# Performance work log

Hardware: AMD Instinct MI355X
Metric: run time of the kernel (lower is better)

## Reference

```python
import math
import jax, jax.numpy as jnp
import numpy as np

L, D, H, F = 4, 1024, 16, 4096
HD = D // H
EPS = 1e-5


def get_alibi_slopes(num_heads):
    closest = 2 ** math.floor(math.log2(num_heads))
    base = 2 ** (-2 ** (-(math.log2(closest) - 3)))
    slopes = base ** np.arange(1, closest + 1)
    if closest != num_heads:
        extra_base = 2 ** (-2 ** (-(math.log2(2 * closest) - 3)))
        extra = extra_base ** np.arange(1, 2 * (num_heads - closest) + 1, 2)
        slopes = np.concatenate([slopes, extra])
    return jnp.asarray(slopes, dtype=jnp.float32)


def build_mask(num_heads, T):
    # causal: -inf above diagonal; plus ALiBi slopes * (key_pos - query_pos)
    pos = jnp.arange(T)
    dist = pos[None, :] - pos[:, None]                      # (T, T)
    alibi = get_alibi_slopes(num_heads)[:, None, None] * dist[None]  # (H, T, T)
    causal = jnp.where(dist > 0, -jnp.inf, 0.0).astype(jnp.float32)
    return causal[None] + alibi                             # (H, T, T)


def layer_norm(x, w, b):
    mu = jnp.mean(x, axis=-1, keepdims=True)
    var = jnp.mean(jnp.square(x - mu), axis=-1, keepdims=True)
    return (x - mu) * jax.lax.rsqrt(var + EPS) * w + b


def mha(x, mask, Wi, bi, Wo, bo):
    B, T, _ = x.shape
    qkv = x @ Wi.T + bi                                     # (B, T, 3D)
    q, k, v = jnp.split(qkv, 3, axis=-1)
    q = q.reshape(B, T, H, HD).transpose(0, 2, 1, 3)        # (B, H, T, hd)
    k = k.reshape(B, T, H, HD).transpose(0, 2, 1, 3)
    v = v.reshape(B, T, H, HD).transpose(0, 2, 1, 3)
    scores = jnp.einsum('bhqd,bhkd->bhqk', q, k) / math.sqrt(HD)
    scores = scores + mask[None]                            # (B, H, T, T)
    attn = jax.nn.softmax(scores, axis=-1)
    out = jnp.einsum('bhqk,bhkd->bhqd', attn, v)
    out = out.transpose(0, 2, 1, 3).reshape(B, T, D)
    return out @ Wo.T + bo


def setup_inputs() -> dict:
    key = jax.random.key(0)
    ks = jax.random.split(key, 13)
    s = 0.02
    inp = {
        'x': jax.random.normal(ks[0], (2, 2048, D), dtype=jnp.float32),
        'in_proj_w': jax.random.normal(ks[1], (L, 3 * D, D), dtype=jnp.float32) * s,
        'in_proj_b': jnp.zeros((L, 3 * D), dtype=jnp.float32),
        'out_proj_w': jax.random.normal(ks[2], (L, D, D), dtype=jnp.float32) * s,
        'out_proj_b': jnp.zeros((L, D), dtype=jnp.float32),
        'ffn1_w': jax.random.normal(ks[3], (L, F, D), dtype=jnp.float32) * s,
        'ffn1_b': jnp.zeros((L, F), dtype=jnp.float32),
        'ffn2_w': jax.random.normal(ks[4], (L, D, F), dtype=jnp.float32) * s,
        'ffn2_b': jnp.zeros((L, D), dtype=jnp.float32),
        'ln1_w': jnp.ones((L, D), dtype=jnp.float32),
        'ln1_b': jnp.zeros((L, D), dtype=jnp.float32),
        'ln2_w': jnp.ones((L, D), dtype=jnp.float32),
        'ln2_b': jnp.zeros((L, D), dtype=jnp.float32),
        'final_w': jnp.ones((D,), dtype=jnp.float32),
        'final_b': jnp.zeros((D,), dtype=jnp.float32),
    }
    return inp


def reference(x, in_proj_w, in_proj_b, out_proj_w, out_proj_b,
              ffn1_w, ffn1_b, ffn2_w, ffn2_b,
              ln1_w, ln1_b, ln2_w, ln2_b, final_w, final_b):
    T = x.shape[1]
    mask = build_mask(H, T)                                 # (H, T, T)
    for i in range(L):
        xn = layer_norm(x, ln1_w[i], ln1_b[i])
        x = x + mha(xn, mask, in_proj_w[i], in_proj_b[i], out_proj_w[i], out_proj_b[i])
        xn = layer_norm(x, ln2_w[i], ln2_b[i])
        h = jax.nn.gelu(xn @ ffn1_w[i].T + ffn1_b[i], approximate=False)
        x = x + (h @ ffn2_w[i].T + ffn2_b[i])
    return layer_norm(x, final_w, final_b)
```

## Files before the change

kernel.cpp:

```cpp
#include <hip/hip_runtime.h>
#include <hip/hip_bf16.h>
#include <math.h>

typedef __bf16 bf16x8 __attribute__((ext_vector_type(8)));
typedef __bf16 bf16x4 __attribute__((ext_vector_type(4)));
typedef float  floatx4 __attribute__((ext_vector_type(4)));

#define D_MODEL 1024
#define SEQ     2048
#define NHEAD   16
#define HD      64

__device__ __forceinline__ void async16(const void* g, void* l) {
  __builtin_amdgcn_global_load_lds((const __attribute__((address_space(1))) void*)g,
                                   (__attribute__((address_space(3))) void*)l, 16, 0, 0);
}

__global__ __launch_bounds__(256)
void cvtw_kernel(const float* __restrict__ in, __bf16* __restrict__ out) {
  const size_t i = ((size_t)blockIdx.x * 256 + threadIdx.x) * 4;
  const floatx4 f = *(const floatx4*)(in + i);
  bf16x4 o = { (__bf16)f[0], (__bf16)f[1], (__bf16)f[2], (__bf16)f[3] };
  *(bf16x4*)(out + i) = o;
}

template<bool OUT_BF16>
__global__ __launch_bounds__(256)
void ln_kernel(const float* __restrict__ x, const float* __restrict__ w,
               const float* __restrict__ b, void* __restrict__ out)
{
  const int row = blockIdx.x;
  const int tid = threadIdx.x;
  const floatx4 f = *(const floatx4*)(x + (size_t)row * D_MODEL + tid * 4);
  float s = f[0] + f[1] + f[2] + f[3];
  #pragma unroll
  for (int off = 1; off < 64; off <<= 1) s += __shfl_xor(s, off);
  __shared__ float red[8];
  const int wv = tid >> 6;
  if ((tid & 63) == 0) red[wv] = s;
  __syncthreads();
  const float mu = (red[0] + red[1] + red[2] + red[3]) * (1.0f / 1024.0f);
  float d0 = f[0] - mu, d1 = f[1] - mu, d2 = f[2] - mu, d3 = f[3] - mu;
  float ss = d0 * d0 + d1 * d1 + d2 * d2 + d3 * d3;
  #pragma unroll
  for (int off = 1; off < 64; off <<= 1) ss += __shfl_xor(ss, off);
  if ((tid & 63) == 0) red[4 + wv] = ss;
  __syncthreads();
  const float rstd = rsqrtf((red[4] + red[5] + red[6] + red[7]) * (1.0f / 1024.0f) + 1e-5f);
  const floatx4 wv4 = *(const floatx4*)(w + tid * 4);
  const floatx4 bv4 = *(const floatx4*)(b + tid * 4);
  const float y0 = d0 * rstd * wv4[0] + bv4[0];
  const float y1 = d1 * rstd * wv4[1] + bv4[1];
  const float y2 = d2 * rstd * wv4[2] + bv4[2];
  const float y3 = d3 * rstd * wv4[3] + bv4[3];
  if (OUT_BF16) {
    bf16x4 o = { (__bf16)y0, (__bf16)y1, (__bf16)y2, (__bf16)y3 };
    *(bf16x4*)((__bf16*)out + (size_t)row * D_MODEL + tid * 4) = o;
  } else {
    floatx4 o = { y0, y1, y2, y3 };
    *(floatx4*)((float*)out + (size_t)row * D_MODEL + tid * 4) = o;
  }
}

#define EPI_GELU 1
#define EPI_RES  2
#define EPI_QKV  3

__device__ __forceinline__ void stage_tile(const __bf16* Ab, const __bf16* Wb,
                                           int K, int k0,
                                           __bf16 (*As)[64], __bf16 (*Bs)[64], int tid)
{
  #pragma unroll
  for (int j = 0; j < 4; ++j) {
    const int ch = j * 512 + tid;
    const int row = ch >> 3, c16 = ch & 7;
    const int gc = (c16 ^ (row & 7)) * 8;
    async16(Ab + (size_t)row * K + k0 + gc, &As[row][c16 * 8]);
  }
  #pragma unroll
  for (int j = 0; j < 4; ++j) {
    const int ch = j * 512 + tid;
    const int row = ch >> 3, c16 = ch & 7;
    const int gc = (c16 ^ (row & 7)) * 8;
    async16(Wb + (size_t)row * K + k0 + gc, &Bs[row][c16 * 8]);
  }
}

template<int MODE>
__global__ __launch_bounds__(512, 2)
void gemm256_kernel(const __bf16* __restrict__ A, const __bf16* __restrict__ W,
                    const float* __restrict__ bias, void* out,
                    __bf16* __restrict__ vT, int M, int N, int K)
{
  __shared__ __align__(16) __bf16 As[2][256][64];
  __shared__ __align__(16) __bf16 Bs[2][256][64];
  const int tid = threadIdx.x;
  const int lane = tid & 63, wv = tid >> 6;
  const int wr = wv >> 2, wc = wv & 3;
  const int quad = lane >> 4, r = lane & 15;
  const int sw = r & 7;
  const int m0 = blockIdx.x * 256, n0 = blockIdx.y * 256;
  const __bf16* Ab = A + (size_t)m0 * K;
  const __bf16* Wb = W + (size_t)n0 * K;

  floatx4 acc[8][4] = {};

  const int nt = K >> 6;
  stage_tile(Ab, Wb, K, 0, As[0], Bs[0], tid);

  for (int t = 0; t < nt; ++t) {
    const int p = t & 1;
    const int kn = (t + 1 < nt) ? ((t + 1) << 6) : 0;
    stage_tile(Ab, Wb, K, kn, As[p ^ 1], Bs[p ^ 1], tid);
    asm volatile("s_waitcnt vmcnt(8)" ::: "memory");
    __builtin_amdgcn_s_barrier();
    asm volatile("" ::: "memory");
    __bf16 (*Asr)[64] = As[p];
    __bf16 (*Bsr)[64] = Bs[p];
    #pragma unroll
    for (int kk = 0; kk < 2; ++kk) {
      const int cc = ((kk * 4 + quad) ^ sw) * 8;
      bf16x8 av[8], bv[4];
      #pragma unroll
      for (int mi = 0; mi < 8; ++mi)
        av[mi] = *(const bf16x8*)&Asr[wr * 128 + mi * 16 + r][cc];
      #pragma unroll
      for (int ni = 0; ni < 4; ++ni)
        bv[ni] = *(const bf16x8*)&Bsr[wc * 64 + ni * 16 + r][cc];
      __builtin_amdgcn_s_setprio(1);
      #pragma unroll
      for (int ni = 0; ni < 4; ++ni)
        #pragma unroll
        for (int mi = 0; mi < 8; ++mi)
          acc[mi][ni] = __builtin_amdgcn_mfma_f32_16x16x32_bf16(
              av[mi], bv[ni], acc[mi][ni], 0, 0, 0);
      __builtin_amdgcn_s_setprio(0);
    }
    asm volatile("" ::: "memory");
    __builtin_amdgcn_s_barrier();
  }
  asm volatile("s_waitcnt vmcnt(0)" ::: "memory");

  #pragma unroll
  for (int ni = 0; ni < 4; ++ni) {
    const int nn = n0 + wc * 64 + ni * 16 + r;
    const float bvv = bias[nn];
    #pragma unroll
    for (int mi = 0; mi < 8; ++mi) {
      #pragma unroll
      for (int v = 0; v < 4; ++v) {
        const int mm = m0 + wr * 128 + mi * 16 + quad * 4 + v;
        float val = acc[mi][ni][v] + bvv;
        if (MODE == EPI_GELU) {
          val = 0.5f * val * (1.0f + erff(val * 0.70710678118654752f));
          ((__bf16*)out)[(size_t)mm * N + nn] = (__bf16)val;
        } else if (MODE == EPI_QKV) {
          if (nn < 2048) {
            const float sv = (nn < 1024) ? val * 0.125f : val;
            ((__bf16*)out)[(size_t)mm * 2048 + nn] = (__bf16)sv;
          } else {
            const int c = nn - 2048, hh = c >> 6, dd = c & 63;
            const int bb = mm >> 11, tt = mm & 2047;
            vT[(size_t)((bb * 16 + hh) * 64 + dd) * 2048 + tt] = (__bf16)val;
          }
        }
      }
    }
  }
}

__global__ __launch_bounds__(256, 2)
void gemm64_kernel(const __bf16* __restrict__ A, const __bf16* __restrict__ W,
                   const float* __restrict__ bias, float* __restrict__ out,
                   const float* __restrict__ res, int M, int N, int K)
{
  __shared__ __align__(16) __bf16 As0[128][32], As1[128][32];
  __shared__ __align__(16) __bf16 Ws0[64][32],  Ws1[64][32];
  const int tid = threadIdx.x;
  const int lane = tid & 63, w = tid >> 6;
  const int wr = w >> 1, wc = w & 1;
  const int quad = lane >> 4, r = lane & 15;
  const int m0 = blockIdx.x * 128, n0 = blockIdx.y * 64;

  floatx4 acc[4][2] = {};

  const __bf16* Ab = A + (size_t)m0 * K;
  const __bf16* Wb = W + (size_t)n0 * K;
  const int sr = tid >> 2, sc = (tid & 3) * 8;

  for (int k0 = 0; k0 < K; k0 += 64) {
    async16(Ab + (size_t)sr * K + k0 + sc,             &As0[sr][sc]);
    async16(Ab + (size_t)(sr + 64) * K + k0 + sc,      &As0[sr + 64][sc]);
    async16(Ab + (size_t)sr * K + k0 + 32 + sc,        &As1[sr][sc]);
    async16(Ab + (size_t)(sr + 64) * K + k0 + 32 + sc, &As1[sr + 64][sc]);
    async16(Wb + (size_t)sr * K + k0 + sc,             &Ws0[sr][sc]);
    async16(Wb + (size_t)sr * K + k0 + 32 + sc,        &Ws1[sr][sc]);
    __syncthreads();
    bf16x8 af0[4], af1[4];
    #pragma unroll
    for (int mi = 0; mi < 4; ++mi) {
      af0[mi] = *(const bf16x8*)&As0[wr * 64 + mi * 16 + r][quad * 8];
      af1[mi] = *(const bf16x8*)&As1[wr * 64 + mi * 16 + r][quad * 8];
    }
    #pragma unroll
    for (int ni = 0; ni < 2; ++ni) {
      const bf16x8 b0 = *(const bf16x8*)&Ws0[wc * 32 + ni * 16 + r][quad * 8];
      const bf16x8 b1 = *(const bf16x8*)&Ws1[wc * 32 + ni * 16 + r][quad * 8];
      #pragma unroll
      for (int mi = 0; mi < 4; ++mi) {
        acc[mi][ni] = __builtin_amdgcn_mfma_f32_16x16x32_bf16(af0[mi], b0, acc[mi][ni], 0, 0, 0);
        acc[mi][ni] = __builtin_amdgcn_mfma_f32_16x16x32_bf16(af1[mi], b1, acc[mi][ni], 0, 0, 0);
      }
    }
    __syncthreads();
  }

  #pragma unroll
  for (int ni = 0; ni < 2; ++ni) {
    const int nn = n0 + wc * 32 + ni * 16 + r;
    const float bv = bias[nn];
    #pragma unroll
    for (int mi = 0; mi < 4; ++mi) {
      #pragma unroll
      for (int v = 0; v < 4; ++v) {
        const int mm = m0 + wr * 64 + mi * 16 + quad * 4 + v;
        out[(size_t)mm * N + nn] = res[(size_t)mm * N + nn] + acc[mi][ni][v] + bv;
      }
    }
  }
}

template<int MODE, int NT>
__global__ __launch_bounds__(256, 2)
void gemm_legacy_kernel(const __bf16* __restrict__ A, const float* __restrict__ W,
                        const float* __restrict__ bias, void* out,
                        const float* __restrict__ res, __bf16* __restrict__ vT,
                        int M, int N, int K)
{
  __shared__ __align__(16) __bf16 As[128][32];
  __shared__ __align__(16) __bf16 Ws[NT][32];
  const int tid = threadIdx.x;
  const int lane = tid & 63, w = tid >> 6;
  const int wr = w >> 1, wc = w & 1;
  const int quad = lane >> 4, r = lane & 15;
  constexpr int NACC = NT / 32;
  const int m0 = blockIdx.x * 128, n0 = blockIdx.y * NT;
  floatx4 acc[4][NACC] = {};
  const __bf16* Ab = A + (size_t)m0 * K;
  const float*  Wb = W + (size_t)n0 * K;
  const int arow = tid >> 2, ac = (tid & 3) * 8;
  const int wrow = tid >> 3, wc4 = (tid & 7) * 4;
  for (int k0 = 0; k0 < K; k0 += 32) {
    async16(Ab + (size_t)arow * K + k0 + ac, &As[arow][ac]);
    async16(Ab + (size_t)(arow + 64) * K + k0 + ac, &As[arow + 64][ac]);
    #pragma unroll
    for (int i = 0; i < NT / 32; ++i) {
      const int rw = wrow + 32 * i;
      const floatx4 f = *(const floatx4*)(Wb + (size_t)rw * K + k0 + wc4);
      bf16x4 h4 = { (__bf16)f[0], (__bf16)f[1], (__bf16)f[2], (__bf16)f[3] };
      *(bf16x4*)&Ws[rw][wc4] = h4;
    }
    __syncthreads();
    bf16x8 af[4];
    #pragma unroll
    for (int mi = 0; mi < 4; ++mi)
      af[mi] = *(const bf16x8*)&As[wr * 64 + mi * 16 + r][quad * 8];
    #pragma unroll
    for (int ni = 0; ni < NACC; ++ni) {
      bf16x8 bf = *(const bf16x8*)&Ws[wc * (NT / 2) + ni * 16 + r][quad * 8];
      #pragma unroll
      for (int mi = 0; mi < 4; ++mi)
        acc[mi][ni] = __builtin_amdgcn_mfma_f32_16x16x32_bf16(af[mi], bf, acc[mi][ni], 0, 0, 0);
    }
    __syncthreads();
  }
  #pragma unroll
  for (int ni = 0; ni < NACC; ++ni) {
    const int nn = n0 + wc * (NT / 2) + ni * 16 + r;
    const float bv = bias[nn];
    #pragma unroll
    for (int mi = 0; mi < 4; ++mi) {
      #pragma unroll
      for (int v = 0; v < 4; ++v) {
        const int mm = m0 + wr * 64 + mi * 16 + quad * 4 + v;
        float val = acc[mi][ni][v] + bv;
        if (MODE == EPI_GELU) {
          val = 0.5f * val * (1.0f + erff(val * 0.70710678118654752f));
          ((__bf16*)out)[(size_t)mm * N + nn] = (__bf16)val;
        } else if (MODE == EPI_RES) {
          ((float*)out)[(size_t)mm * N + nn] = res[(size_t)mm * N + nn] + val;
        } else if (MODE == EPI_QKV) {
          if (nn < 2048) {
            const float sv = (nn < 1024) ? val * 0.125f : val;
            ((__bf16*)out)[(size_t)mm * 2048 + nn] = (__bf16)sv;
          } else {
            const int c = nn - 2048, hh = c >> 6, dd = c & 63;
            const int bb = mm >> 11, t = mm & 2047;
            vT[(size_t)((bb * 16 + hh) * 64 + dd) * 2048 + t] = (__bf16)val;
          }
        }
      }
    }
  }
}

__global__ __launch_bounds__(256, 4)
void attn_kernel(const __bf16* __restrict__ qk,
                 const __bf16* __restrict__ vT,
                 __bf16* __restrict__ out)
{
  __shared__ __align__(16) __bf16 Qs[2][64][32];
  __shared__ __align__(16) __bf16 Ks[2][64][32];
  __shared__ __align__(16) __bf16 Vs[2][64][32];
  __shared__ __align__(16) __bf16 Ps[4][2][16][32];
  const int tid = threadIdx.x, lane = tid & 63, w = tid >> 6;
  const int quad = lane >> 4, r = lane & 15;
  const int bh = blockIdx.x, b = bh >> 4, h = bh & 15;
  const int yk = blockIdx.y >> 3, yj = blockIdx.y & 7;
  const int qt = (yk << 3) | ((yk & 1) ? (7 - yj) : yj);
  const int q0 = qt * 64;

  {
    const __bf16* qb = qk + ((size_t)(b * SEQ + q0)) * 2048 + h * 64;
    #pragma unroll
    for (int rd = 0; rd < 2; ++rd) {
      const int c = rd * 256 + tid, half = c >> 8, row = (c >> 2) & 63, c8 = (c & 3) * 8;
      async16(qb + (size_t)row * 2048 + half * 32 + c8, &Qs[half][row][c8]);
    }
  }
  __syncthreads();
  const bf16x8 qf0 = *(const bf16x8*)&Qs[0][w * 16 + r][quad * 8];
  const bf16x8 qf1 = *(const bf16x8*)&Qs[1][w * 16 + r][quad * 8];

  const int q = q0 + w * 16 + r;
  float m_i = -INFINITY, l_i = 0.0f;
  floatx4 ot[4] = {};
  const float slope = exp2f(-0.5f * (float)(h + 1));
  const float sq = slope * (float)q;

  const __bf16* kb0 = qk + ((size_t)(b * SEQ)) * 2048 + 1024 + h * 64;
  const __bf16* vb0 = vT + ((size_t)(bh * 64)) * 2048;

  for (int kt = 0; kt <= qt; ++kt) {
    const int kbase = kt << 6;
    #pragma unroll
    for (int rd = 0; rd < 2; ++rd) {
      const int c = rd * 256 + tid, half = c >> 8, row = (c >> 2) & 63, c8 = (c & 3) * 8;
      async16(kb0 + (size_t)(kbase + row) * 2048 + half * 32 + c8, &Ks[half][row][c8]);
    }
    #pragma unroll
    for (int rd = 0; rd < 2; ++rd) {
      const int c = rd * 256 + tid, kb = c >> 8, d = (c >> 2) & 63, c8 = (c & 3) * 8;
      async16(vb0 + (size_t)d * 2048 + kbase + kb * 32 + c8, &Vs[kb][d][c8]);
    }
    __syncthreads();

    floatx4 st[4];
    #pragma unroll
    for (int t = 0; t < 4; ++t) {
      floatx4 z = { 0.0f, 0.0f, 0.0f, 0.0f };
      const bf16x8 kf0 = *(const bf16x8*)&Ks[0][t * 16 + r][quad * 8];
      const bf16x8 kf1 = *(const bf16x8*)&Ks[1][t * 16 + r][quad * 8];
      z = __builtin_amdgcn_mfma_f32_16x16x32_bf16(kf0, qf0, z, 0, 0, 0);
      st[t] = __builtin_amdgcn_mfma_f32_16x16x32_bf16(kf1, qf1, z, 0, 0, 0);
    }
    float mloc = -INFINITY;
    if (kt == qt) {
      #pragma unroll
      for (int t = 0; t < 4; ++t)
        #pragma unroll
        for (int v = 0; v < 4; ++v) {
          const int key = kbase + t * 16 + quad * 4 + v;
          float sv = st[t][v] + slope * (float)key - sq;
          sv = (key <= q) ? sv : -INFINITY;
          st[t][v] = sv;
          mloc = fmaxf(mloc, sv);
        }
    } else {
      #pragma unroll
      for (int t = 0; t < 4; ++t)
        #pragma unroll
        for (int v = 0; v < 4; ++v) {
          const int key = kbase + t * 16 + quad * 4 + v;
          const float sv = st[t][v] + slope * (float)key - sq;
          st[t][v] = sv;
          mloc = fmaxf(mloc, sv);
        }
    }
    mloc = fmaxf(mloc, __shfl_xor(mloc, 16));
    mloc = fmaxf(mloc, __shfl_xor(mloc, 32));
    const float mn = fmaxf(m_i, mloc);
    const float alpha = __expf(m_i - mn);
    m_i = mn;
    float rsum = 0.0f;
    #pragma unroll
    for (int t = 0; t < 4; ++t) {
      bf16x4 p4;
      #pragma unroll
      for (int v = 0; v < 4; ++v) {
        const float p = __expf(st[t][v] - mn);
        rsum += p;
        p4[v] = (__bf16)p;
      }
      *(bf16x4*)&Ps[w][t >> 1][r][(t & 1) * 16 + quad * 4] = p4;
    }
    rsum += __shfl_xor(rsum, 16);
    rsum += __shfl_xor(rsum, 32);
    l_i = l_i * alpha + rsum;
    #pragma unroll
    for (int dt = 0; dt < 4; ++dt) ot[dt] *= alpha;

    #pragma unroll
    for (int kb = 0; kb < 2; ++kb) {
      const bf16x8 pf = *(const bf16x8*)&Ps[w][kb][r][quad * 8];
      #pragma unroll
      for (int dt = 0; dt < 4; ++dt) {
        const bf16x8 vf = *(const bf16x8*)&Vs[kb][dt * 16 + r][quad * 8];
        ot[dt] = __builtin_amdgcn_mfma_f32_16x16x32_bf16(vf, pf, ot[dt], 0, 0, 0);
      }
    }
    __syncthreads();
  }

  const float linv = 1.0f / l_i;
  __bf16* ob = out + (size_t)(b * SEQ + q) * D_MODEL + h * 64;
  #pragma unroll
  for (int dt = 0; dt < 4; ++dt) {
    bf16x4 o4 = { (__bf16)(ot[dt][0] * linv), (__bf16)(ot[dt][1] * linv),
                  (__bf16)(ot[dt][2] * linv), (__bf16)(ot[dt][3] * linv) };
    *(bf16x4*)(ob + dt * 16 + quad * 4) = o4;
  }
}

extern "C" void kernel_launch(void* const* d_in, const int* in_sizes, int n_in,
                              void* d_out, int out_size, void* d_ws, size_t ws_size,
                              hipStream_t stream)
{
  (void)in_sizes; (void)n_in; (void)out_size;
  const float* x    = (const float*)d_in[0];
  const float* inW  = (const float*)d_in[1];
  const float* inB  = (const float*)d_in[2];
  const float* outW = (const float*)d_in[3];
  const float* outB = (const float*)d_in[4];
  const float* f1W  = (const float*)d_in[5];
  const float* f1B  = (const float*)d_in[6];
  const float* f2W  = (const float*)d_in[7];
  const float* f2B  = (const float*)d_in[8];
  const float* ln1W = (const float*)d_in[9];
  const float* ln1B = (const float*)d_in[10];
  const float* ln2W = (const float*)d_in[11];
  const float* ln2B = (const float*)d_in[12];
  const float* fnW  = (const float*)d_in[13];
  const float* fnB  = (const float*)d_in[14];

  char* ws = (char*)d_ws;
  float*  x_cur = (float*)(ws);
  __bf16* xn    = (__bf16*)(ws + 16777216);
  __bf16* qk    = (__bf16*)(ws + 25165824);
  __bf16* vT    = (__bf16*)(ws + 41943040);
  __bf16* attn  = (__bf16*)(ws + 50331648);
  __bf16* hbuf  = (__bf16*)(ws + 25165824);
  __bf16* inWb  = (__bf16*)(ws + 58720256);
  __bf16* outWb = (__bf16*)(ws + 83886080);
  __bf16* f1Wb  = (__bf16*)(ws + 92274688);
  __bf16* f2Wb  = (__bf16*)(ws + 125829120);
  const bool bf16w = ws_size >= (size_t)159383552;

  hipMemcpyAsync(x_cur, x, (size_t)16777216, hipMemcpyDeviceToDevice, stream);

  if (bf16w) {
    cvtw_kernel<<<dim3(12288), dim3(256), 0, stream>>>(inW,  inWb);
    cvtw_kernel<<<dim3(4096),  dim3(256), 0, stream>>>(outW, outWb);
    cvtw_kernel<<<dim3(16384), dim3(256), 0, stream>>>(f1W,  f1Wb);
    cvtw_kernel<<<dim3(16384), dim3(256), 0, stream>>>(f2W,  f2Wb);
  }

  for (int i = 0; i < 4; ++i) {
    ln_kernel<true><<<dim3(4096), dim3(256), 0, stream>>>(
        x_cur, ln1W + i * 1024, ln1B + i * 1024, xn);
    if (bf16w)
      gemm256_kernel<EPI_QKV><<<dim3(16, 12), dim3(512), 0, stream>>>(
          xn, inWb + (size_t)i * 3072 * 1024, inB + (size_t)i * 3072,
          qk, vT, 4096, 3072, 1024);
    else
      gemm_legacy_kernel<EPI_QKV, 128><<<dim3(32, 24), dim3(256), 0, stream>>>(
          xn, inW + (size_t)i * 3072 * 1024, inB + (size_t)i * 3072,
          qk, nullptr, vT, 4096, 3072, 1024);
    attn_kernel<<<dim3(32, 32), dim3(256), 0, stream>>>(qk, vT, attn);
    if (bf16w)
      gemm64_kernel<<<dim3(32, 16), dim3(256), 0, stream>>>(
          attn, outWb + (size_t)i * 1024 * 1024, outB + (size_t)i * 1024,
          x_cur, x_cur, 4096, 1024, 1024);
    else
      gemm_legacy_kernel<EPI_RES, 64><<<dim3(32, 16), dim3(256), 0, stream>>>(
          attn, outW + (size_t)i * 1024 * 1024, outB + (size_t)i * 1024,
          x_cur, x_cur, nullptr, 4096, 1024, 1024);
    ln_kernel<true><<<dim3(4096), dim3(256), 0, stream>>>(
        x_cur, ln2W + i * 1024, ln2B + i * 1024, xn);
    if (bf16w)
      gemm256_kernel<EPI_GELU><<<dim3(16, 16), dim3(512), 0, stream>>>(
          xn, f1Wb + (size_t)i * 4096 * 1024, f1B + (size_t)i * 4096,
          hbuf, nullptr, 4096, 4096, 1024);
    else
      gemm_legacy_kernel<EPI_GELU, 128><<<dim3(32, 32), dim3(256), 0, stream>>>(
          xn, f1W + (size_t)i * 4096 * 1024, f1B + (size_t)i * 4096,
          hbuf, nullptr, nullptr, 4096, 4096, 1024);
    if (bf16w)
      gemm64_kernel<<<dim3(32, 16), dim3(256), 0, stream>>>(
          hbuf, f2Wb + (size_t)i * 1024 * 4096, f2B + (size_t)i * 1024,
          x_cur, x_cur, 4096, 1024, 4096);
    else
      gemm_legacy_kernel<EPI_RES, 64><<<dim3(32, 16), dim3(256), 0, stream>>>(
          hbuf, f2W + (size_t)i * 1024 * 4096, f2B + (size_t)i * 1024,
          x_cur, x_cur, nullptr, 4096, 1024, 4096);
  }
  ln_kernel<false><<<dim3(4096), dim3(256), 0, stream>>>(x_cur, fnW, fnB, d_out);
}
```

Measured before the change: 1.350 ms.

## Interleave split prefetch with quarter-tile MFMA phases and stage epilogue through LDS

Each K step of the 256x256 bf16 GEMM is split into four MFMA quadrants separated by barriers. The A and W tile prefetches are issued between these phases, so global-to-LDS loads overlap the matrix math and register fragments are reused across quadrants. The epilogue now writes results into LDS and stores coalesced 16-byte vectors, including a transposed staging path for the V output, replacing scattered 2-byte global stores. This adds barriers per K step and per epilogue pass, and relies on syncthreads to make the async loads visible.

```diff
diff --git a/kernel.cpp b/kernel.cpp
--- a/kernel.cpp
+++ b/kernel.cpp
@@ -66,34 +66,16 @@
 #define EPI_RES  2
 #define EPI_QKV  3
 
-__device__ __forceinline__ void stage_tile(const __bf16* Ab, const __bf16* Wb,
-                                           int K, int k0,
-                                           __bf16 (*As)[64], __bf16 (*Bs)[64], int tid)
-{
-  #pragma unroll
-  for (int j = 0; j < 4; ++j) {
-    const int ch = j * 512 + tid;
-    const int row = ch >> 3, c16 = ch & 7;
-    const int gc = (c16 ^ (row & 7)) * 8;
-    async16(Ab + (size_t)row * K + k0 + gc, &As[row][c16 * 8]);
-  }
-  #pragma unroll
-  for (int j = 0; j < 4; ++j) {
-    const int ch = j * 512 + tid;
-    const int row = ch >> 3, c16 = ch & 7;
-    const int gc = (c16 ^ (row & 7)) * 8;
-    async16(Wb + (size_t)row * K + k0 + gc, &Bs[row][c16 * 8]);
-  }
-}
-
 template<int MODE>
 __global__ __launch_bounds__(512, 2)
 void gemm256_kernel(const __bf16* __restrict__ A, const __bf16* __restrict__ W,
                     const float* __restrict__ bias, void* out,
                     __bf16* __restrict__ vT, int M, int N, int K)
 {
-  __shared__ __align__(16) __bf16 As[2][256][64];
-  __shared__ __align__(16) __bf16 Bs[2][256][64];
+  __shared__ __align__(16) char smem[131072];
+  __bf16 (*As)[256][64] = reinterpret_cast<__bf16 (*)[256][64]>(smem);
+  __bf16 (*Bs)[256][64] = reinterpret_cast<__bf16 (*)[256][64]>(smem + 65536);
+
   const int tid = threadIdx.x;
   const int lane = tid & 63, wv = tid >> 6;
   const int wr = wv >> 2, wc = wv & 3;
@@ -106,66 +88,186 @@
   floatx4 acc[8][4] = {};
 
   const int nt = K >> 6;
-  stage_tile(Ab, Wb, K, 0, As[0], Bs[0], tid);
+
+  #pragma unroll
+  for (int j = 0; j < 4; ++j) {
+    const int ch = j * 512 + tid;
+    const int row = ch >> 3, c16 = ch & 7;
+    const int gcb = (c16 ^ (row & 7)) * 8;
+    async16(Ab + (size_t)row * K + gcb, &As[0][row][c16 * 8]);
+  }
+  #pragma unroll
+  for (int j = 0; j < 4; ++j) {
+    const int ch = j * 512 + tid;
+    const int row = ch >> 3, c16 = ch & 7;
+    const int gcb = (c16 ^ (row & 7)) * 8;
+    async16(Wb + (size_t)row * K + gcb, &Bs[0][row][c16 * 8]);
+  }
+  __syncthreads();
 
   for (int t = 0; t < nt; ++t) {
-    const int p = t & 1;
-    const int kn = (t + 1 < nt) ? ((t + 1) << 6) : 0;
-    stage_tile(Ab, Wb, K, kn, As[p ^ 1], Bs[p ^ 1], tid);
-    asm volatile("s_waitcnt vmcnt(8)" ::: "memory");
+    const int pr = t & 1;
+    const __bf16 (*Asr)[64] = As[pr];
+    const __bf16 (*Bsr)[64] = Bs[pr];
+    const bool pf = (t + 1 < nt);
+    const int kn = (t + 1) << 6;
+
+    bf16x8 a0[2][4], b0[2][2], b1[2][2];
+
+    if (pf) {
+      #pragma unroll
+      for (int j = 0; j < 4; ++j) {
+        const int ch = j * 512 + tid;
+        const int row = ch >> 3, c16 = ch & 7;
+        const int gcb = (c16 ^ (row & 7)) * 8;
+        async16(Ab + (size_t)row * K + kn + gcb, &As[pr ^ 1][row][c16 * 8]);
+      }
+    }
+    #pragma unroll
+    for (int kk = 0; kk < 2; ++kk) {
+      const int cc = ((kk * 4 + quad) ^ sw) * 8;
+      #pragma unroll
+      for (int mi = 0; mi < 4; ++mi)
+        a0[kk][mi] = *(const bf16x8*)&Asr[wr * 128 + mi * 16 + r][cc];
+      #pragma unroll
+      for (int ni = 0; ni < 2; ++ni)
+        b0[kk][ni] = *(const bf16x8*)&Bsr[wc * 64 + ni * 16 + r][cc];
+    }
+    __builtin_amdgcn_s_setprio(1);
+    #pragma unroll
+    for (int kk = 0; kk < 2; ++kk)
+      #pragma unroll
+      for (int ni = 0; ni < 2; ++ni)
+        #pragma unroll
+        for (int mi = 0; mi < 4; ++mi)
+          acc[mi][ni] = __builtin_amdgcn_mfma_f32_16x16x32_bf16(
+              a0[kk][mi], b0[kk][ni], acc[mi][ni], 0, 0, 0);
+    __builtin_amdgcn_s_setprio(0);
+    asm volatile("" ::: "memory");
     __builtin_amdgcn_s_barrier();
     asm volatile("" ::: "memory");
-    __bf16 (*Asr)[64] = As[p];
-    __bf16 (*Bsr)[64] = Bs[p];
+
+    if (pf) {
+      #pragma unroll
+      for (int j = 0; j < 4; ++j) {
+        const int ch = j * 512 + tid;
+        const int row = ch >> 3, c16 = ch & 7;
+        const int gcb = (c16 ^ (row & 7)) * 8;
+        async16(Wb + (size_t)row * K + kn + gcb, &Bs[pr ^ 1][row][c16 * 8]);
+      }
+    }
     #pragma unroll
     for (int kk = 0; kk < 2; ++kk) {
       const int cc = ((kk * 4 + quad) ^ sw) * 8;
-      bf16x8 av[8], bv[4];
-      #pragma unroll
-      for (int mi = 0; mi < 8; ++mi)
-        av[mi] = *(const bf16x8*)&Asr[wr * 128 + mi * 16 + r][cc];
-      #pragma unroll
-      for (int ni = 0; ni < 4; ++ni)
-        bv[ni] = *(const bf16x8*)&Bsr[wc * 64 + ni * 16 + r][cc];
-      __builtin_amdgcn_s_setprio(1);
-      #pragma unroll
-      for (int ni = 0; ni < 4; ++ni)
+      #pragma unroll
+      for (int ni = 0; ni < 2; ++ni)
+        b1[kk][ni] = *(const bf16x8*)&Bsr[wc * 64 + 32 + ni * 16 + r][cc];
+    }
+    __builtin_amdgcn_s_setprio(1);
+    #pragma unroll
+    for (int kk = 0; kk < 2; ++kk)
+      #pragma unroll
+      for (int ni = 0; ni < 2; ++ni)
         #pragma unroll
-        for (int mi = 0; mi < 8; ++mi)
-          acc[mi][ni] = __builtin_amdgcn_mfma_f32_16x16x32_bf16(
-              av[mi], bv[ni], acc[mi][ni], 0, 0, 0);
-      __builtin_amdgcn_s_setprio(0);
-    }
+        for (int mi = 0; mi < 4; ++mi)
+          acc[mi][2 + ni] = __builtin_amdgcn_mfma_f32_16x16x32_bf16(
+              a0[kk][mi], b1[kk][ni], acc[mi][2 + ni], 0, 0, 0);
+    __builtin_amdgcn_s_setprio(0);
     asm volatile("" ::: "memory");
     __builtin_amdgcn_s_barrier();
-  }
-  asm volatile("s_waitcnt vmcnt(0)" ::: "memory");
-
-  #pragma unroll
-  for (int ni = 0; ni < 4; ++ni) {
-    const int nn = n0 + wc * 64 + ni * 16 + r;
-    const float bvv = bias[nn];
-    #pragma unroll
-    for (int mi = 0; mi < 8; ++mi) {
-      #pragma unroll
-      for (int v = 0; v < 4; ++v) {
-        const int mm = m0 + wr * 128 + mi * 16 + quad * 4 + v;
-        float val = acc[mi][ni][v] + bvv;
-        if (MODE == EPI_GELU) {
-          val = 0.5f * val * (1.0f + erff(val * 0.70710678118654752f));
-          ((__bf16*)out)[(size_t)mm * N + nn] = (__bf16)val;
-        } else if (MODE == EPI_QKV) {
-          if (nn < 2048) {
-            const float sv = (nn < 1024) ? val * 0.125f : val;
-            ((__bf16*)out)[(size_t)mm * 2048 + nn] = (__bf16)sv;
+    asm volatile("" ::: "memory");
+
+    #pragma unroll
+    for (int kk = 0; kk < 2; ++kk) {
+      const int cc = ((kk * 4 + quad) ^ sw) * 8;
+      #pragma unroll
+      for (int mi = 0; mi < 4; ++mi)
+        a0[kk][mi] = *(const bf16x8*)&Asr[wr * 128 + 64 + mi * 16 + r][cc];
+    }
+    __builtin_amdgcn_s_setprio(1);
+    #pragma unroll
+    for (int kk = 0; kk < 2; ++kk)
+      #pragma unroll
+      for (int ni = 0; ni < 2; ++ni)
+        #pragma unroll
+        for (int mi = 0; mi < 4; ++mi)
+          acc[4 + mi][2 + ni] = __builtin_amdgcn_mfma_f32_16x16x32_bf16(
+              a0[kk][mi], b1[kk][ni], acc[4 + mi][2 + ni], 0, 0, 0);
+    __builtin_amdgcn_s_setprio(0);
+    asm volatile("" ::: "memory");
+    __builtin_amdgcn_s_barrier();
+    asm volatile("" ::: "memory");
+
+    __builtin_amdgcn_s_setprio(1);
+    #pragma unroll
+    for (int kk = 0; kk < 2; ++kk)
+      #pragma unroll
+      for (int ni = 0; ni < 2; ++ni)
+        #pragma unroll
+        for (int mi = 0; mi < 4; ++mi)
+          acc[4 + mi][ni] = __builtin_amdgcn_mfma_f32_16x16x32_bf16(
+              a0[kk][mi], b0[kk][ni], acc[4 + mi][ni], 0, 0, 0);
+    __builtin_amdgcn_s_setprio(0);
+    __syncthreads();
+  }
+
+  __bf16 (*Cs)[264] = reinterpret_cast<__bf16 (*)[264]>(smem);
+  __bf16 (*Ct)[136] = reinterpret_cast<__bf16 (*)[136]>(smem);
+  const bool vblock = (MODE == EPI_QKV) && (n0 >= 2048);
+  const size_t ostride = (MODE == EPI_QKV) ? (size_t)2048 : (size_t)N;
+
+  #pragma unroll
+  for (int pass = 0; pass < 2; ++pass) {
+    if (wr == pass) {
+      #pragma unroll
+      for (int ni = 0; ni < 4; ++ni) {
+        const int nn_l = wc * 64 + ni * 16 + r;
+        const float bvv = bias[n0 + nn_l];
+        #pragma unroll
+        for (int mi = 0; mi < 8; ++mi) {
+          if (vblock) {
+            bf16x4 o4;
+            #pragma unroll
+            for (int v = 0; v < 4; ++v) o4[v] = (__bf16)(acc[mi][ni][v] + bvv);
+            *(bf16x4*)&Ct[nn_l][mi * 16 + quad * 4] = o4;
           } else {
-            const int c = nn - 2048, hh = c >> 6, dd = c & 63;
-            const int bb = mm >> 11, tt = mm & 2047;
-            vT[(size_t)((bb * 16 + hh) * 64 + dd) * 2048 + tt] = (__bf16)val;
+            #pragma unroll
+            for (int v = 0; v < 4; ++v) {
+              float val = acc[mi][ni][v] + bvv;
+              if (MODE == EPI_GELU)
+                val = 0.5f * val * (1.0f + erff(val * 0.70710678118654752f));
+              if (MODE == EPI_QKV && (n0 + nn_l) < 1024) val *= 0.125f;
+              Cs[mi * 16 + quad * 4 + v][nn_l] = (__bf16)val;
+            }
           }
         }
       }
     }
+    __syncthreads();
+    if (vblock) {
+      const int c0 = n0 - 2048;
+      const int bb = m0 >> 11;
+      #pragma unroll
+      for (int rd = 0; rd < 8; ++rd) {
+        const int idx = rd * 512 + tid;
+        const int rn = idx >> 4, ch = idx & 15;
+        const bf16x8 o = *(const bf16x8*)&Ct[rn][ch * 8];
+        const int c = c0 + rn, hh = c >> 6, dd = c & 63;
+        const int tt = (m0 & 2047) + pass * 128 + ch * 8;
+        *(bf16x8*)(vT + ((size_t)((bb * 16 + hh) * 64 + dd)) * 2048 + tt) = o;
+      }
+    } else {
+      #pragma unroll
+      for (int rd = 0; rd < 8; ++rd) {
+        const int idx = rd * 512 + tid;
+        const int rowm = idx >> 5, ch = idx & 31;
+        const bf16x8 o = *(const bf16x8*)&Cs[rowm][ch * 8];
+        const int mm = m0 + pass * 128 + rowm;
+        const int nn = n0 + ch * 8;
+        *(bf16x8*)((__bf16*)out + (size_t)mm * ostride + nn) = o;
+      }
+    }
+    __syncthreads();
   }
 }
 
```

Result: faster. 1.269 ms (-6.0%).

## Replace 256x256 pipelined GEMM with 128x128 tile GEMM and LDS-staged epilogue

Applied to the files above, without the earlier changes.

Swaps the double-buffered, swizzled 256x256-tile GEMM used for the QKV and FFN1 projections for a simpler 128x128-tile, single-buffered kernel with K-step 32, and launches more blocks. The epilogue now goes through shared memory so output rows, and the transposed V tile, are written with 16-byte vectorized stores instead of scattered 2-byte stores. The aim is better grid occupancy (more blocks across the CUs) and coalesced output writes. In exchange it gives up the double-buffer overlap and the per-tile data reuse of the larger tile, and adds more synchronisation per K-step.

```diff
diff --git a/kernel.cpp b/kernel.cpp
--- a/kernel.cpp
+++ b/kernel.cpp
@@ -66,106 +66,104 @@
 #define EPI_RES  2
 #define EPI_QKV  3
 
-__device__ __forceinline__ void stage_tile(const __bf16* Ab, const __bf16* Wb,
-                                           int K, int k0,
-                                           __bf16 (*As)[64], __bf16 (*Bs)[64], int tid)
-{
-  #pragma unroll
-  for (int j = 0; j < 4; ++j) {
-    const int ch = j * 512 + tid;
-    const int row = ch >> 3, c16 = ch & 7;
-    const int gc = (c16 ^ (row & 7)) * 8;
-    async16(Ab + (size_t)row * K + k0 + gc, &As[row][c16 * 8]);
-  }
-  #pragma unroll
-  for (int j = 0; j < 4; ++j) {
-    const int ch = j * 512 + tid;
-    const int row = ch >> 3, c16 = ch & 7;
-    const int gc = (c16 ^ (row & 7)) * 8;
-    async16(Wb + (size_t)row * K + k0 + gc, &Bs[row][c16 * 8]);
-  }
-}
-
 template<int MODE>
-__global__ __launch_bounds__(512, 2)
-void gemm256_kernel(const __bf16* __restrict__ A, const __bf16* __restrict__ W,
+__global__ __launch_bounds__(256, 2)
+void gemm128_kernel(const __bf16* __restrict__ A, const __bf16* __restrict__ W,
                     const float* __restrict__ bias, void* out,
                     __bf16* __restrict__ vT, int M, int N, int K)
 {
-  __shared__ __align__(16) __bf16 As[2][256][64];
-  __shared__ __align__(16) __bf16 Bs[2][256][64];
+  __shared__ __align__(16) char smem[18432];
+  __bf16 (*As)[32] = reinterpret_cast<__bf16 (*)[32]>(smem);
+  __bf16 (*Ws)[32] = reinterpret_cast<__bf16 (*)[32]>(smem + 8192);
   const int tid = threadIdx.x;
-  const int lane = tid & 63, wv = tid >> 6;
-  const int wr = wv >> 2, wc = wv & 3;
+  const int lane = tid & 63, w = tid >> 6;
+  const int wr = w >> 1, wc = w & 1;
   const int quad = lane >> 4, r = lane & 15;
-  const int sw = r & 7;
-  const int m0 = blockIdx.x * 256, n0 = blockIdx.y * 256;
+  const int m0 = blockIdx.x * 128, n0 = blockIdx.y * 128;
+
+  floatx4 acc[4][4] = {};
+
   const __bf16* Ab = A + (size_t)m0 * K;
   const __bf16* Wb = W + (size_t)n0 * K;
-
-  floatx4 acc[8][4] = {};
-
-  const int nt = K >> 6;
-  stage_tile(Ab, Wb, K, 0, As[0], Bs[0], tid);
-
-  for (int t = 0; t < nt; ++t) {
-    const int p = t & 1;
-    const int kn = (t + 1 < nt) ? ((t + 1) << 6) : 0;
-    stage_tile(Ab, Wb, K, kn, As[p ^ 1], Bs[p ^ 1], tid);
-    asm volatile("s_waitcnt vmcnt(8)" ::: "memory");
-    __builtin_amdgcn_s_barrier();
-    asm volatile("" ::: "memory");
-    __bf16 (*Asr)[64] = As[p];
-    __bf16 (*Bsr)[64] = Bs[p];
-    #pragma unroll
-    for (int kk = 0; kk < 2; ++kk) {
-      const int cc = ((kk * 4 + quad) ^ sw) * 8;
-      bf16x8 av[8], bv[4];
-      #pragma unroll
-      for (int mi = 0; mi < 8; ++mi)
-        av[mi] = *(const bf16x8*)&Asr[wr * 128 + mi * 16 + r][cc];
-      #pragma unroll
-      for (int ni = 0; ni < 4; ++ni)
-        bv[ni] = *(const bf16x8*)&Bsr[wc * 64 + ni * 16 + r][cc];
-      __builtin_amdgcn_s_setprio(1);
-      #pragma unroll
-      for (int ni = 0; ni < 4; ++ni)
+  const int sr = tid >> 2, sc = (tid & 3) * 8;
+
+  for (int k0 = 0; k0 < K; k0 += 32) {
+    async16(Ab + (size_t)sr * K + k0 + sc, &As[sr][sc]);
+    async16(Ab + (size_t)(sr + 64) * K + k0 + sc, &As[sr + 64][sc]);
+    async16(Wb + (size_t)sr * K + k0 + sc, &Ws[sr][sc]);
+    async16(Wb + (size_t)(sr + 64) * K + k0 + sc, &Ws[sr + 64][sc]);
+    __syncthreads();
+    bf16x8 af[4];
+    #pragma unroll
+    for (int mi = 0; mi < 4; ++mi)
+      af[mi] = *(const bf16x8*)&As[wr * 64 + mi * 16 + r][quad * 8];
+    #pragma unroll
+    for (int ni = 0; ni < 4; ++ni) {
+      const bf16x8 bf = *(const bf16x8*)&Ws[wc * 64 + ni * 16 + r][quad * 8];
+      #pragma unroll
+      for (int mi = 0; mi < 4; ++mi)
+        acc[mi][ni] = __builtin_amdgcn_mfma_f32_16x16x32_bf16(af[mi], bf, acc[mi][ni], 0, 0, 0);
+    }
+    __syncthreads();
+  }
+
+  __bf16 (*Cs)[136] = reinterpret_cast<__bf16 (*)[136]>(smem);
+  __bf16 (*Ct)[72]  = reinterpret_cast<__bf16 (*)[72]>(smem);
+  const bool vblock = (MODE == EPI_QKV) && (n0 >= 2048);
+  const size_t ostride = (MODE == EPI_QKV) ? (size_t)2048 : (size_t)N;
+
+  #pragma unroll
+  for (int pass = 0; pass < 2; ++pass) {
+    if (wr == pass) {
+      #pragma unroll
+      for (int ni = 0; ni < 4; ++ni) {
+        const int nn_l = wc * 64 + ni * 16 + r;
+        const float bvv = bias[n0 + nn_l];
         #pragma unroll
-        for (int mi = 0; mi < 8; ++mi)
-          acc[mi][ni] = __builtin_amdgcn_mfma_f32_16x16x32_bf16(
-              av[mi], bv[ni], acc[mi][ni], 0, 0, 0);
-      __builtin_amdgcn_s_setprio(0);
-    }
-    asm volatile("" ::: "memory");
-    __builtin_amdgcn_s_barrier();
-  }
-  asm volatile("s_waitcnt vmcnt(0)" ::: "memory");
-
-  #pragma unroll
-  for (int ni = 0; ni < 4; ++ni) {
-    const int nn = n0 + wc * 64 + ni * 16 + r;
-    const float bvv = bias[nn];
-    #pragma unroll
-    for (int mi = 0; mi < 8; ++mi) {
-      #pragma unroll
-      for (int v = 0; v < 4; ++v) {
-        const int mm = m0 + wr * 128 + mi * 16 + quad * 4 + v;
-        float val = acc[mi][ni][v] + bvv;
-        if (MODE == EPI_GELU) {
-          val = 0.5f * val * (1.0f + erff(val * 0.70710678118654752f));
-          ((__bf16*)out)[(size_t)mm * N + nn] = (__bf16)val;
-        } else if (MODE == EPI_QKV) {
-          if (nn < 2048) {
-            const float sv = (nn < 1024) ? val * 0.125f : val;
-            ((__bf16*)out)[(size_t)mm * 2048 + nn] = (__bf16)sv;
+        for (int mi = 0; mi < 4; ++mi) {
+          if (vblock) {
+            bf16x4 o4;
+            #pragma unroll
+            for (int v = 0; v < 4; ++v) o4[v] = (__bf16)(acc[mi][ni][v] + bvv);
+            *(bf16x4*)&Ct[nn_l][mi * 16 + quad * 4] = o4;
           } else {
-            const int c = nn - 2048, hh = c >> 6, dd = c & 63;
-            const int bb = mm >> 11, tt = mm & 2047;
-            vT[(size_t)((bb * 16 + hh) * 64 + dd) * 2048 + tt] = (__bf16)val;
+            #pragma unroll
+            for (int v = 0; v < 4; ++v) {
+              float val = acc[mi][ni][v] + bvv;
+              if (MODE == EPI_GELU)
+                val = 0.5f * val * (1.0f + erff(val * 0.70710678118654752f));
+              if (MODE == EPI_QKV && (n0 + nn_l) < 1024) val *= 0.125f;
+              Cs[mi * 16 + quad * 4 + v][nn_l] = (__bf16)val;
+            }
           }
         }
       }
     }
+    __syncthreads();
+    if (vblock) {
+      const int c0 = n0 - 2048;
+      const int bb = m0 >> 11;
+      #pragma unroll
+      for (int rd = 0; rd < 4; ++rd) {
+        const int idx = rd * 256 + tid;
+        const int rn = idx >> 3, ch = idx & 7;
+        const bf16x8 o = *(const bf16x8*)&Ct[rn][ch * 8];
+        const int c = c0 + rn, hh = c >> 6, dd = c & 63;
+        const int tt = (m0 & 2047) + pass * 64 + ch * 8;
+        *(bf16x8*)(vT + ((size_t)((bb * 16 + hh) * 64 + dd)) * 2048 + tt) = o;
+      }
+    } else {
+      #pragma unroll
+      for (int rd = 0; rd < 4; ++rd) {
+        const int idx = rd * 256 + tid;
+        const int rowm = idx >> 4, ch = idx & 15;
+        const bf16x8 o = *(const bf16x8*)&Cs[rowm][ch * 8];
+        const int mm = m0 + pass * 64 + rowm;
+        const int nn = n0 + ch * 8;
+        *(bf16x8*)((__bf16*)out + (size_t)mm * ostride + nn) = o;
+      }
+    }
+    __syncthreads();
   }
 }
 
@@ -479,7 +477,7 @@
     ln_kernel<true><<<dim3(4096), dim3(256), 0, stream>>>(
         x_cur, ln1W + i * 1024, ln1B + i * 1024, xn);
     if (bf16w)
-      gemm256_kernel<EPI_QKV><<<dim3(16, 12), dim3(512), 0, stream>>>(
+      gemm128_kernel<EPI_QKV><<<dim3(32, 24), dim3(256), 0, stream>>>(
           xn, inWb + (size_t)i * 3072 * 1024, inB + (size_t)i * 3072,
           qk, vT, 4096, 3072, 1024);
     else
@@ -498,7 +496,7 @@
     ln_kernel<true><<<dim3(4096), dim3(256), 0, stream>>>(
         x_cur, ln2W + i * 1024, ln2B + i * 1024, xn);
     if (bf16w)
-      gemm256_kernel<EPI_GELU><<<dim3(16, 16), dim3(512), 0, stream>>>(
+      gemm128_kernel<EPI_GELU><<<dim3(32, 32), dim3(256), 0, stream>>>(
           xn, f1Wb + (size_t)i * 4096 * 1024, f1B + (size_t)i * 4096,
           hbuf, nullptr, 4096, 4096, 1024);
     else
```

Measured after the change: 1.239 ms. 8.2% less time.
